# Kernel optimization log

Measured on AMD Instinct MI355X. Metric: run time of the kernel, lower is better.

The kernel has to match this reference:

```python
import jax, jax.numpy as jnp
import numpy as np
from math import sqrt

N, D = 8192, 64

def setup_inputs() -> dict:
    key = jax.random.key(0)
    kq, kk, kv = jax.random.split(key, 3)
    q = jax.random.normal(kq, (N, D), dtype=jnp.float32)
    k = jax.random.normal(kk, (N, D), dtype=jnp.float32)
    v = jax.random.normal(kv, (N, D), dtype=jnp.float32)
    return {"q": q, "k": k, "v": v}

def reference(q, k, v):
    # Mathematically identical to the block-wise online-softmax loop:
    # after processing all KV blocks, m_blk == rowmax(S), l_blk == rowsum(exp(S - m)),
    # O = (exp(S - m) @ V) / l.
    scale = 1.0 / sqrt(q.shape[-1])
    S = (q @ k.T) * scale            # [N, N] attention scores
    m = jnp.max(S, axis=1, keepdims=True)   # running max -> global row max
    P = jnp.exp(S - m)                      # unnormalized probs
    L = jnp.sum(P, axis=1, keepdims=True)   # softmax denominator, [N, 1]
    O = (P @ v) / L                          # [N, D]
    return (O, L)
```

## Files before the change

kernel.cpp:

```cpp
#include <hip/hip_runtime.h>
#include <hip/hip_bf16.h>
#include <math.h>

#define N 8192
#define D 64
#define QSCALE 0.18033688011112042f

typedef __attribute__((ext_vector_type(8))) short short8;
typedef __attribute__((ext_vector_type(16))) float f32x16;

__device__ inline short f32_to_bf16_bits(float x) {
    union { float f; unsigned u; } c; c.f = x;
    unsigned u = c.u;
    u += 0x7FFFu + ((u >> 16) & 1u);
    return (short)(u >> 16);
}
__device__ inline float bfbits_to_f32(unsigned short u) {
    union { unsigned u; float f; } c; c.u = ((unsigned)u) << 16;
    return c.f;
}
__device__ inline unsigned cvt_pk_bf16(float a, float b) {
    __hip_bfloat162 h = __float22bfloat162_rn(make_float2(a, b));
    union { __hip_bfloat162 h; unsigned u; } c; c.h = h;
    return c.u;
}

__global__ __launch_bounds__(256) void fa_conv(const float* __restrict__ q,
                                               const float* __restrict__ k,
                                               const float* __restrict__ v,
                                               short* __restrict__ Qb,
                                               short* __restrict__ Kp,
                                               short* __restrict__ Vp) {
    int bid = blockIdx.x, tid = threadIdx.x;
    if (bid < 512) {
        int i = (bid * 256 + tid) * 4;
        float4 a = *(const float4*)(q + i);
        unsigned lo = cvt_pk_bf16(a.x * QSCALE, a.y * QSCALE);
        unsigned hi = cvt_pk_bf16(a.z * QSCALE, a.w * QSCALE);
        unsigned long long u = (unsigned long long)lo | ((unsigned long long)hi << 32);
        *(unsigned long long*)(Qb + i) = u;
    } else if (bid < 768) {
        int t = bid - 512;
        int c = tid >> 6, l = tid & 63, ql = l & 31, hi = l >> 5;
        const float* src = k + (size_t)(t * 32 + ql) * D + c * 16 + hi * 8;
        float4 a = *(const float4*)(src);
        float4 b = *(const float4*)(src + 4);
        uint4 u = { cvt_pk_bf16(a.x, a.y), cvt_pk_bf16(a.z, a.w),
                    cvt_pk_bf16(b.x, b.y), cvt_pk_bf16(b.z, b.w) };
        *(uint4*)(Kp + (size_t)t * 2048 + c * 512 + ql * 16 + hi * 8) = u;
    } else {
        int t = bid - 768;
        int dt = tid >> 7, h = (tid >> 6) & 1, ql = (tid >> 1) & 31, hi = tid & 1;
        int col = dt * 32 + ql;
        const float* src = v + (size_t)(t * 32 + h * 16 + hi * 8) * D + col;
        float f[8];
#pragma unroll
        for (int j = 0; j < 8; ++j) f[j] = src[(size_t)j * D];
        uint4 u = { cvt_pk_bf16(f[0], f[1]), cvt_pk_bf16(f[2], f[3]),
                    cvt_pk_bf16(f[4], f[5]), cvt_pk_bf16(f[6], f[7]) };
        *(uint4*)(Vp + (size_t)t * 2048 + dt * 1024 + h * 512 + ql * 16 + hi * 8) = u;
    }
}

__global__ __launch_bounds__(256) void fa_part_kernel(const short* __restrict__ Qb,
                                                      const short* __restrict__ Kp,
                                                      const short* __restrict__ Vp,
                                                      short* __restrict__ OTb,
                                                      float* __restrict__ Ml,
                                                      int KN) {
    const int qt = blockIdx.x & 63;
    const int s  = blockIdx.x >> 6;
    const int w = threadIdx.x >> 6, lane = threadIdx.x & 63;
    const int ql = lane & 31, hi = lane >> 5;
    const int qrow = qt * 128 + w * 32 + ql;

    const short* qp = Qb + (size_t)qrow * D + hi * 8;
    short8 qf0 = *(const short8*)(qp);
    short8 qf1 = *(const short8*)(qp + 16);
    short8 qf2 = *(const short8*)(qp + 32);
    short8 qf3 = *(const short8*)(qp + 48);

    f32x16 acc0 = {}, acc1 = {};
    float mex = -INFINITY, lsum = 0.f;

    const int t0 = (s * KN) >> 5, nt = KN >> 5;
    const short* kb = Kp + (size_t)t0 * 2048 + ql * 16 + hi * 8;
    const short* vb = Vp + (size_t)t0 * 2048 + ql * 16 + hi * 8;

#pragma unroll 1
    for (int t = 0; t < nt; ++t) {
        const short* kp = kb + (size_t)t * 2048;
        const short* vp = vb + (size_t)t * 2048;
        short8 kf0  = *(const short8*)(kp);
        short8 kf1  = *(const short8*)(kp + 512);
        short8 kf2  = *(const short8*)(kp + 1024);
        short8 kf3  = *(const short8*)(kp + 1536);
        short8 vf00 = *(const short8*)(vp);
        short8 vf01 = *(const short8*)(vp + 512);
        short8 vf10 = *(const short8*)(vp + 1024);
        short8 vf11 = *(const short8*)(vp + 1536);

        __builtin_amdgcn_s_setprio(1);
        f32x16 st = {};
        st = __builtin_amdgcn_mfma_f32_32x32x16_bf16(kf0, qf0, st, 0, 0, 0);
        st = __builtin_amdgcn_mfma_f32_32x32x16_bf16(kf1, qf1, st, 0, 0, 0);
        st = __builtin_amdgcn_mfma_f32_32x32x16_bf16(kf2, qf2, st, 0, 0, 0);
        st = __builtin_amdgcn_mfma_f32_32x32x16_bf16(kf3, qf3, st, 0, 0, 0);
        __builtin_amdgcn_s_setprio(0);

        float g0 = fmaxf(fmaxf(st[0], st[1]), st[2]);
        float g1 = fmaxf(fmaxf(st[3], st[4]), st[5]);
        float g2 = fmaxf(fmaxf(st[6], st[7]), st[8]);
        float g3 = fmaxf(fmaxf(st[9], st[10]), st[11]);
        float g4 = fmaxf(fmaxf(st[12], st[13]), st[14]);
        float t5 = fmaxf(fmaxf(g0, g1), g2);
        float t6 = fmaxf(fmaxf(g3, g4), st[15]);
        mex = fmaxf(mex, fmaxf(t5, t6));

        unsigned pk0, pk1, pk2, pk3, pk4, pk5, pk6, pk7;
        float rs;
        {
            float a, b;
            a = __builtin_amdgcn_exp2f(st[0]);  b = __builtin_amdgcn_exp2f(st[1]);
            rs = a + b;            pk0 = cvt_pk_bf16(a, b);
            a = __builtin_amdgcn_exp2f(st[2]);  b = __builtin_amdgcn_exp2f(st[3]);
            rs += a + b;           pk1 = cvt_pk_bf16(a, b);
            a = __builtin_amdgcn_exp2f(st[4]);  b = __builtin_amdgcn_exp2f(st[5]);
            rs += a + b;           pk2 = cvt_pk_bf16(a, b);
            a = __builtin_amdgcn_exp2f(st[6]);  b = __builtin_amdgcn_exp2f(st[7]);
            rs += a + b;           pk3 = cvt_pk_bf16(a, b);
            a = __builtin_amdgcn_exp2f(st[8]);  b = __builtin_amdgcn_exp2f(st[9]);
            rs += a + b;           pk4 = cvt_pk_bf16(a, b);
            a = __builtin_amdgcn_exp2f(st[10]); b = __builtin_amdgcn_exp2f(st[11]);
            rs += a + b;           pk5 = cvt_pk_bf16(a, b);
            a = __builtin_amdgcn_exp2f(st[12]); b = __builtin_amdgcn_exp2f(st[13]);
            rs += a + b;           pk6 = cvt_pk_bf16(a, b);
            a = __builtin_amdgcn_exp2f(st[14]); b = __builtin_amdgcn_exp2f(st[15]);
            rs += a + b;           pk7 = cvt_pk_bf16(a, b);
        }
        lsum += rs;

        auto r0 = __builtin_amdgcn_permlane32_swap((int)pk0, (int)pk2, false, false);
        auto r1 = __builtin_amdgcn_permlane32_swap((int)pk1, (int)pk3, false, false);
        auto r2 = __builtin_amdgcn_permlane32_swap((int)pk4, (int)pk6, false, false);
        auto r3 = __builtin_amdgcn_permlane32_swap((int)pk5, (int)pk7, false, false);
        union { int i[4]; short8 s8; } pb0, pb1;
        pb0.i[0] = r0[0]; pb0.i[1] = r1[0]; pb0.i[2] = r0[1]; pb0.i[3] = r1[1];
        pb1.i[0] = r2[0]; pb1.i[1] = r3[0]; pb1.i[2] = r2[1]; pb1.i[3] = r3[1];

        __builtin_amdgcn_s_setprio(1);
        acc0 = __builtin_amdgcn_mfma_f32_32x32x16_bf16(vf00, pb0.s8, acc0, 0, 0, 0);
        acc0 = __builtin_amdgcn_mfma_f32_32x32x16_bf16(vf01, pb1.s8, acc0, 0, 0, 0);
        acc1 = __builtin_amdgcn_mfma_f32_32x32x16_bf16(vf10, pb0.s8, acc1, 0, 0, 0);
        acc1 = __builtin_amdgcn_mfma_f32_32x32x16_bf16(vf11, pb1.s8, acc1, 0, 0, 0);
        __builtin_amdgcn_s_setprio(0);
    }

    mex = fmaxf(mex, __shfl_xor(mex, 32));
    lsum += __shfl_xor(lsum, 32);

#pragma unroll
    for (int r = 0; r < 16; ++r) {
        int d0 = (r & 3) + 8 * (r >> 2) + 4 * hi;
        OTb[(size_t)(s * 64 + d0) * N + qrow]      = f32_to_bf16_bits(acc0[r]);
        OTb[(size_t)(s * 64 + 32 + d0) * N + qrow] = f32_to_bf16_bits(acc1[r]);
    }
    if (hi == 0) {
        Ml[(size_t)(s * 2 + 0) * N + qrow] = lsum;
        Ml[(size_t)(s * 2 + 1) * N + qrow] = mex;
    }
}

__global__ __launch_bounds__(256) void fa_comb_kernel(const short* __restrict__ OTb,
                                                      const float* __restrict__ Ml,
                                                      float* __restrict__ Out, int S) {
    const int r0 = blockIdx.x * 64;
    const int row = threadIdx.x & 63, db = threadIdx.x >> 6;
    const int grow = r0 + row;

    float v[16];
#pragma unroll
    for (int i = 0; i < 16; ++i) v[i] = 0.f;
    float L = 0.f, mg = -INFINITY;
    for (int s = 0; s < S; ++s) {
#pragma unroll
        for (int i = 0; i < 16; ++i)
            v[i] += bfbits_to_f32((unsigned short)OTb[(size_t)(s * 64 + db * 16 + i) * N + grow]);
        L  += Ml[(size_t)(s * 2 + 0) * N + grow];
        mg = fmaxf(mg, Ml[(size_t)(s * 2 + 1) * N + grow]);
    }
    float inv = 1.0f / L;
    float4* outv = (float4*)(Out + (size_t)grow * D + db * 16);
#pragma unroll
    for (int i4 = 0; i4 < 4; ++i4) {
        float4 o = { v[i4 * 4 + 0] * inv, v[i4 * 4 + 1] * inv,
                     v[i4 * 4 + 2] * inv, v[i4 * 4 + 3] * inv };
        outv[i4] = o;
    }
    if (db == 0) Out[(size_t)N * D + grow] = exp2f(-mg) * L;
}

extern "C" void kernel_launch(void* const* d_in, const int* in_sizes, int n_in,
                              void* d_out, int out_size, void* d_ws, size_t ws_size,
                              hipStream_t stream) {
    const float* q = (const float*)d_in[0];
    const float* k = (const float*)d_in[1];
    const float* v = (const float*)d_in[2];
    float* out = (float*)d_out;

    short* Qb = (short*)d_ws;
    short* Kp = Qb + (size_t)N * D;
    short* Vp = Kp + (size_t)N * D;
    short* OTb = (short*)((char*)d_ws + 3 * 1048576);

    int S = 16;
    while (S > 1 &&
           3ull * 1048576 + (size_t)S * (64ull * N * 2) + (size_t)S * (2ull * N * 4) > ws_size)
        S >>= 1;
    float* Ml = (float*)(OTb + (size_t)S * 64 * N);
    int KN = N / S;

    fa_conv<<<1024, 256, 0, stream>>>(q, k, v, Qb, Kp, Vp);
    fa_part_kernel<<<64 * S, 256, 0, stream>>>(Qb, Kp, Vp, OTb, Ml, KN);
    fa_comb_kernel<<<N / 64, 256, 0, stream>>>(OTb, Ml, out, S);
}
```

Baseline: 50.12 us.

## Stage K/V tiles through double-buffered LDS with global_load_lds prefetch

Instead of each wave loading K and V fragments straight from global memory, the block cooperatively copies 64-key K/V tiles into a double-buffered LDS array with global_load_lds, prefetching the next tile while computing on the current one. The conversion kernel's packed layout is changed to a lane-contiguous order so each lane's 16-byte LDS read and each 16-byte global_load_lds line up. The aim is to stop the four waves from each fetching the same K/V data and to hide global latency. In exchange it adds a block-wide barrier and vmcnt wait per tile, uses 32 KB of LDS, and removes the setprio hints.

```diff
diff --git a/kernel.cpp b/kernel.cpp
--- a/kernel.cpp
+++ b/kernel.cpp
@@ -24,6 +24,11 @@
     union { __hip_bfloat162 h; unsigned u; } c; c.h = h;
     return c.u;
 }
+
+#define GLDS(gp, lp)                                                            \
+    __builtin_amdgcn_global_load_lds(                                           \
+        (const __attribute__((address_space(1))) void*)(gp),                    \
+        (__attribute__((address_space(3))) void*)(lp), 16, 0, 0)
 
 __global__ __launch_bounds__(256) void fa_conv(const float* __restrict__ q,
                                                const float* __restrict__ k,
@@ -47,18 +52,17 @@
         float4 b = *(const float4*)(src + 4);
         uint4 u = { cvt_pk_bf16(a.x, a.y), cvt_pk_bf16(a.z, a.w),
                     cvt_pk_bf16(b.x, b.y), cvt_pk_bf16(b.z, b.w) };
-        *(uint4*)(Kp + (size_t)t * 2048 + c * 512 + ql * 16 + hi * 8) = u;
+        *(uint4*)(Kp + (size_t)t * 2048 + c * 512 + l * 8) = u;
     } else {
         int t = bid - 768;
-        int dt = tid >> 7, h = (tid >> 6) & 1, ql = (tid >> 1) & 31, hi = tid & 1;
-        int col = dt * 32 + ql;
-        const float* src = v + (size_t)(t * 32 + h * 16 + hi * 8) * D + col;
+        int dt = tid >> 7, h = (tid >> 6) & 1, hi = (tid >> 5) & 1, ql = tid & 31;
+        const float* src = v + (size_t)(t * 32 + h * 16 + hi * 8) * D + dt * 32 + ql;
         float f[8];
 #pragma unroll
         for (int j = 0; j < 8; ++j) f[j] = src[(size_t)j * D];
         uint4 u = { cvt_pk_bf16(f[0], f[1]), cvt_pk_bf16(f[2], f[3]),
                     cvt_pk_bf16(f[4], f[5]), cvt_pk_bf16(f[6], f[7]) };
-        *(uint4*)(Vp + (size_t)t * 2048 + dt * 1024 + h * 512 + ql * 16 + hi * 8) = u;
+        *(uint4*)(Vp + (size_t)t * 2048 + dt * 1024 + h * 512 + hi * 256 + ql * 8) = u;
     }
 }
 
@@ -68,6 +72,9 @@
                                                       short* __restrict__ OTb,
                                                       float* __restrict__ Ml,
                                                       int KN) {
+    __shared__ short Klds[2][4096];
+    __shared__ short Vlds[2][4096];
+
     const int qt = blockIdx.x & 63;
     const int s  = blockIdx.x >> 6;
     const int w = threadIdx.x >> 6, lane = threadIdx.x & 63;
@@ -83,78 +90,98 @@
     f32x16 acc0 = {}, acc1 = {};
     float mex = -INFINITY, lsum = 0.f;
 
-    const int t0 = (s * KN) >> 5, nt = KN >> 5;
-    const short* kb = Kp + (size_t)t0 * 2048 + ql * 16 + hi * 8;
-    const short* vb = Vp + (size_t)t0 * 2048 + ql * 16 + hi * 8;
+    const int T0 = (s * KN) >> 6, nt = KN >> 6;
+    const short* kg = Kp + (size_t)T0 * 4096 + w * 512 + lane * 8;
+    const short* vg = Vp + (size_t)T0 * 4096 + w * 512 + lane * 8;
+
+#define STAGE(buf, T)                                                     \
+    do {                                                                  \
+        const short* kq = kg + (size_t)(T) * 4096;                        \
+        const short* vq = vg + (size_t)(T) * 4096;                        \
+        GLDS(kq,        &Klds[buf][w * 512]);                             \
+        GLDS(kq + 2048, &Klds[buf][2048 + w * 512]);                      \
+        GLDS(vq,        &Vlds[buf][w * 512]);                             \
+        GLDS(vq + 2048, &Vlds[buf][2048 + w * 512]);                      \
+    } while (0)
+
+    STAGE(0, 0);
+    asm volatile("s_waitcnt vmcnt(0)" ::: "memory");
+    __syncthreads();
 
 #pragma unroll 1
-    for (int t = 0; t < nt; ++t) {
-        const short* kp = kb + (size_t)t * 2048;
-        const short* vp = vb + (size_t)t * 2048;
-        short8 kf0  = *(const short8*)(kp);
-        short8 kf1  = *(const short8*)(kp + 512);
-        short8 kf2  = *(const short8*)(kp + 1024);
-        short8 kf3  = *(const short8*)(kp + 1536);
-        short8 vf00 = *(const short8*)(vp);
-        short8 vf01 = *(const short8*)(vp + 512);
-        short8 vf10 = *(const short8*)(vp + 1024);
-        short8 vf11 = *(const short8*)(vp + 1536);
-
-        __builtin_amdgcn_s_setprio(1);
-        f32x16 st = {};
-        st = __builtin_amdgcn_mfma_f32_32x32x16_bf16(kf0, qf0, st, 0, 0, 0);
-        st = __builtin_amdgcn_mfma_f32_32x32x16_bf16(kf1, qf1, st, 0, 0, 0);
-        st = __builtin_amdgcn_mfma_f32_32x32x16_bf16(kf2, qf2, st, 0, 0, 0);
-        st = __builtin_amdgcn_mfma_f32_32x32x16_bf16(kf3, qf3, st, 0, 0, 0);
-        __builtin_amdgcn_s_setprio(0);
-
-        float g0 = fmaxf(fmaxf(st[0], st[1]), st[2]);
-        float g1 = fmaxf(fmaxf(st[3], st[4]), st[5]);
-        float g2 = fmaxf(fmaxf(st[6], st[7]), st[8]);
-        float g3 = fmaxf(fmaxf(st[9], st[10]), st[11]);
-        float g4 = fmaxf(fmaxf(st[12], st[13]), st[14]);
-        float t5 = fmaxf(fmaxf(g0, g1), g2);
-        float t6 = fmaxf(fmaxf(g3, g4), st[15]);
-        mex = fmaxf(mex, fmaxf(t5, t6));
-
-        unsigned pk0, pk1, pk2, pk3, pk4, pk5, pk6, pk7;
-        float rs;
-        {
-            float a, b;
-            a = __builtin_amdgcn_exp2f(st[0]);  b = __builtin_amdgcn_exp2f(st[1]);
-            rs = a + b;            pk0 = cvt_pk_bf16(a, b);
-            a = __builtin_amdgcn_exp2f(st[2]);  b = __builtin_amdgcn_exp2f(st[3]);
-            rs += a + b;           pk1 = cvt_pk_bf16(a, b);
-            a = __builtin_amdgcn_exp2f(st[4]);  b = __builtin_amdgcn_exp2f(st[5]);
-            rs += a + b;           pk2 = cvt_pk_bf16(a, b);
-            a = __builtin_amdgcn_exp2f(st[6]);  b = __builtin_amdgcn_exp2f(st[7]);
-            rs += a + b;           pk3 = cvt_pk_bf16(a, b);
-            a = __builtin_amdgcn_exp2f(st[8]);  b = __builtin_amdgcn_exp2f(st[9]);
-            rs += a + b;           pk4 = cvt_pk_bf16(a, b);
-            a = __builtin_amdgcn_exp2f(st[10]); b = __builtin_amdgcn_exp2f(st[11]);
-            rs += a + b;           pk5 = cvt_pk_bf16(a, b);
-            a = __builtin_amdgcn_exp2f(st[12]); b = __builtin_amdgcn_exp2f(st[13]);
-            rs += a + b;           pk6 = cvt_pk_bf16(a, b);
-            a = __builtin_amdgcn_exp2f(st[14]); b = __builtin_amdgcn_exp2f(st[15]);
-            rs += a + b;           pk7 = cvt_pk_bf16(a, b);
+    for (int T = 0; T < nt; ++T) {
+        const int cur = T & 1;
+        if (T + 1 < nt) STAGE(cur ^ 1, T + 1);
+
+#pragma unroll
+        for (int u = 0; u < 2; ++u) {
+            const short* kt = &Klds[cur][u * 2048];
+            const short* vt = &Vlds[cur][u * 2048];
+            short8 kf0  = *(const short8*)(kt + lane * 8);
+            short8 kf1  = *(const short8*)(kt + 512 + lane * 8);
+            short8 kf2  = *(const short8*)(kt + 1024 + lane * 8);
+            short8 kf3  = *(const short8*)(kt + 1536 + lane * 8);
+            short8 vf00 = *(const short8*)(vt + lane * 8);
+            short8 vf01 = *(const short8*)(vt + 512 + lane * 8);
+            short8 vf10 = *(const short8*)(vt + 1024 + lane * 8);
+            short8 vf11 = *(const short8*)(vt + 1536 + lane * 8);
+
+            f32x16 st = {};
+            st = __builtin_amdgcn_mfma_f32_32x32x16_bf16(kf0, qf0, st, 0, 0, 0);
+            st = __builtin_amdgcn_mfma_f32_32x32x16_bf16(kf1, qf1, st, 0, 0, 0);
+            st = __builtin_amdgcn_mfma_f32_32x32x16_bf16(kf2, qf2, st, 0, 0, 0);
+            st = __builtin_amdgcn_mfma_f32_32x32x16_bf16(kf3, qf3, st, 0, 0, 0);
+
+            float g0 = fmaxf(fmaxf(st[0], st[1]), st[2]);
+            float g1 = fmaxf(fmaxf(st[3], st[4]), st[5]);
+            float g2 = fmaxf(fmaxf(st[6], st[7]), st[8]);
+            float g3 = fmaxf(fmaxf(st[9], st[10]), st[11]);
+            float g4 = fmaxf(fmaxf(st[12], st[13]), st[14]);
+            float t5 = fmaxf(fmaxf(g0, g1), g2);
+            float t6 = fmaxf(fmaxf(g3, g4), st[15]);
+            mex = fmaxf(mex, fmaxf(t5, t6));
+
+            unsigned pk0, pk1, pk2, pk3, pk4, pk5, pk6, pk7;
+            float rs;
+            {
+                float a, b;
+                a = __builtin_amdgcn_exp2f(st[0]);  b = __builtin_amdgcn_exp2f(st[1]);
+                rs = a + b;            pk0 = cvt_pk_bf16(a, b);
+                a = __builtin_amdgcn_exp2f(st[2]);  b = __builtin_amdgcn_exp2f(st[3]);
+                rs += a + b;           pk1 = cvt_pk_bf16(a, b);
+                a = __builtin_amdgcn_exp2f(st[4]);  b = __builtin_amdgcn_exp2f(st[5]);
+                rs += a + b;           pk2 = cvt_pk_bf16(a, b);
+                a = __builtin_amdgcn_exp2f(st[6]);  b = __builtin_amdgcn_exp2f(st[7]);
+                rs += a + b;           pk3 = cvt_pk_bf16(a, b);
+                a = __builtin_amdgcn_exp2f(st[8]);  b = __builtin_amdgcn_exp2f(st[9]);
+                rs += a + b;           pk4 = cvt_pk_bf16(a, b);
+                a = __builtin_amdgcn_exp2f(st[10]); b = __builtin_amdgcn_exp2f(st[11]);
+                rs += a + b;           pk5 = cvt_pk_bf16(a, b);
+                a = __builtin_amdgcn_exp2f(st[12]); b = __builtin_amdgcn_exp2f(st[13]);
+                rs += a + b;           pk6 = cvt_pk_bf16(a, b);
+                a = __builtin_amdgcn_exp2f(st[14]); b = __builtin_amdgcn_exp2f(st[15]);
+                rs += a + b;           pk7 = cvt_pk_bf16(a, b);
+            }
+            lsum += rs;
+
+            auto r0 = __builtin_amdgcn_permlane32_swap((int)pk0, (int)pk2, false, false);
+            auto r1 = __builtin_amdgcn_permlane32_swap((int)pk1, (int)pk3, false, false);
+            auto r2 = __builtin_amdgcn_permlane32_swap((int)pk4, (int)pk6, false, false);
+            auto r3 = __builtin_amdgcn_permlane32_swap((int)pk5, (int)pk7, false, false);
+            union { int i[4]; short8 s8; } pb0, pb1;
+            pb0.i[0] = r0[0]; pb0.i[1] = r1[0]; pb0.i[2] = r0[1]; pb0.i[3] = r1[1];
+            pb1.i[0] = r2[0]; pb1.i[1] = r3[0]; pb1.i[2] = r2[1]; pb1.i[3] = r3[1];
+
+            acc0 = __builtin_amdgcn_mfma_f32_32x32x16_bf16(vf00, pb0.s8, acc0, 0, 0, 0);
+            acc0 = __builtin_amdgcn_mfma_f32_32x32x16_bf16(vf01, pb1.s8, acc0, 0, 0, 0);
+            acc1 = __builtin_amdgcn_mfma_f32_32x32x16_bf16(vf10, pb0.s8, acc1, 0, 0, 0);
+            acc1 = __builtin_amdgcn_mfma_f32_32x32x16_bf16(vf11, pb1.s8, acc1, 0, 0, 0);
         }
-        lsum += rs;
-
-        auto r0 = __builtin_amdgcn_permlane32_swap((int)pk0, (int)pk2, false, false);
-        auto r1 = __builtin_amdgcn_permlane32_swap((int)pk1, (int)pk3, false, false);
-        auto r2 = __builtin_amdgcn_permlane32_swap((int)pk4, (int)pk6, false, false);
-        auto r3 = __builtin_amdgcn_permlane32_swap((int)pk5, (int)pk7, false, false);
-        union { int i[4]; short8 s8; } pb0, pb1;
-        pb0.i[0] = r0[0]; pb0.i[1] = r1[0]; pb0.i[2] = r0[1]; pb0.i[3] = r1[1];
-        pb1.i[0] = r2[0]; pb1.i[1] = r3[0]; pb1.i[2] = r2[1]; pb1.i[3] = r3[1];
-
-        __builtin_amdgcn_s_setprio(1);
-        acc0 = __builtin_amdgcn_mfma_f32_32x32x16_bf16(vf00, pb0.s8, acc0, 0, 0, 0);
-        acc0 = __builtin_amdgcn_mfma_f32_32x32x16_bf16(vf01, pb1.s8, acc0, 0, 0, 0);
-        acc1 = __builtin_amdgcn_mfma_f32_32x32x16_bf16(vf10, pb0.s8, acc1, 0, 0, 0);
-        acc1 = __builtin_amdgcn_mfma_f32_32x32x16_bf16(vf11, pb1.s8, acc1, 0, 0, 0);
-        __builtin_amdgcn_s_setprio(0);
-    }
+
+        asm volatile("s_waitcnt vmcnt(0)" ::: "memory");
+        __syncthreads();
+    }
+#undef STAGE
 
     mex = fmaxf(mex, __shfl_xor(mex, 32));
     lsum += __shfl_xor(lsum, 32);
```

New measurement: 49.90 us. Within noise of the previous version (-0.4%).

## Prefetch next K tile with double-buffered registers and coalesce packed K/V layout

Applied to the files above, without the earlier changes.

Unrolls the KV loop by two and keeps two register sets for K fragments, so the next tile's K loads are issued before the current tile's MFMAs and softmax run. This is meant to hide global-load latency. The packed K/V layout is changed so each lane reads a contiguous lane*8 offset, which makes the 16-byte loads fully coalesced. The row max now uses v_max3_f32 through inline asm. The cost is more registers, and the loop assumes nt is even.

```diff
diff --git a/kernel.cpp b/kernel.cpp
--- a/kernel.cpp
+++ b/kernel.cpp
@@ -23,6 +23,11 @@
     __hip_bfloat162 h = __float22bfloat162_rn(make_float2(a, b));
     union { __hip_bfloat162 h; unsigned u; } c; c.h = h;
     return c.u;
+}
+__device__ inline float max3f(float a, float b, float c) {
+    float d;
+    asm("v_max3_f32 %0, %1, %2, %3" : "=v"(d) : "v"(a), "v"(b), "v"(c));
+    return d;
 }
 
 __global__ __launch_bounds__(256) void fa_conv(const float* __restrict__ q,
@@ -47,18 +52,17 @@
         float4 b = *(const float4*)(src + 4);
         uint4 u = { cvt_pk_bf16(a.x, a.y), cvt_pk_bf16(a.z, a.w),
                     cvt_pk_bf16(b.x, b.y), cvt_pk_bf16(b.z, b.w) };
-        *(uint4*)(Kp + (size_t)t * 2048 + c * 512 + ql * 16 + hi * 8) = u;
+        *(uint4*)(Kp + (size_t)t * 2048 + c * 512 + l * 8) = u;
     } else {
         int t = bid - 768;
-        int dt = tid >> 7, h = (tid >> 6) & 1, ql = (tid >> 1) & 31, hi = tid & 1;
-        int col = dt * 32 + ql;
-        const float* src = v + (size_t)(t * 32 + h * 16 + hi * 8) * D + col;
+        int dt = tid >> 7, h = (tid >> 6) & 1, hi = (tid >> 5) & 1, ql = tid & 31;
+        const float* src = v + (size_t)(t * 32 + h * 16 + hi * 8) * D + dt * 32 + ql;
         float f[8];
 #pragma unroll
         for (int j = 0; j < 8; ++j) f[j] = src[(size_t)j * D];
         uint4 u = { cvt_pk_bf16(f[0], f[1]), cvt_pk_bf16(f[2], f[3]),
                     cvt_pk_bf16(f[4], f[5]), cvt_pk_bf16(f[6], f[7]) };
-        *(uint4*)(Vp + (size_t)t * 2048 + dt * 1024 + h * 512 + ql * 16 + hi * 8) = u;
+        *(uint4*)(Vp + (size_t)t * 2048 + dt * 1024 + h * 512 + hi * 256 + ql * 8) = u;
     }
 }
 
@@ -84,77 +88,91 @@
     float mex = -INFINITY, lsum = 0.f;
 
     const int t0 = (s * KN) >> 5, nt = KN >> 5;
-    const short* kb = Kp + (size_t)t0 * 2048 + ql * 16 + hi * 8;
-    const short* vb = Vp + (size_t)t0 * 2048 + ql * 16 + hi * 8;
-
+    const short* kbp = Kp + (size_t)t0 * 2048 + lane * 8;
+    const short* vbp = Vp + (size_t)t0 * 2048 + lane * 8;
+
+    short8 kA0, kA1, kA2, kA3, kB0, kB1, kB2, kB3;
+    short8 vf0, vf1, vf2, vf3;
+
+#define LOADK(d0, d1, d2, d3, tt) do {                                     \
+        const short* p_ = kbp + (size_t)(tt) * 2048;                       \
+        d0 = *(const short8*)(p_);                                         \
+        d1 = *(const short8*)(p_ + 512);                                   \
+        d2 = *(const short8*)(p_ + 1024);                                  \
+        d3 = *(const short8*)(p_ + 1536);                                  \
+    } while (0)
+#define LOADV(tt) do {                                                     \
+        const short* p_ = vbp + (size_t)(tt) * 2048;                       \
+        vf0 = *(const short8*)(p_);                                        \
+        vf1 = *(const short8*)(p_ + 512);                                  \
+        vf2 = *(const short8*)(p_ + 1024);                                 \
+        vf3 = *(const short8*)(p_ + 1536);                                 \
+    } while (0)
+
+#define TILE(K0, K1, K2, K3) do {                                           \
+        __builtin_amdgcn_s_setprio(1);                                      \
+        f32x16 st = {};                                                     \
+        st = __builtin_amdgcn_mfma_f32_32x32x16_bf16(K0, qf0, st, 0, 0, 0); \
+        st = __builtin_amdgcn_mfma_f32_32x32x16_bf16(K1, qf1, st, 0, 0, 0); \
+        st = __builtin_amdgcn_mfma_f32_32x32x16_bf16(K2, qf2, st, 0, 0, 0); \
+        st = __builtin_amdgcn_mfma_f32_32x32x16_bf16(K3, qf3, st, 0, 0, 0); \
+        __builtin_amdgcn_s_setprio(0);                                      \
+        float m0_ = max3f(st[0], st[1], st[2]);                             \
+        float m1_ = max3f(st[3], st[4], st[5]);                             \
+        float m2_ = max3f(st[6], st[7], st[8]);                             \
+        float m3_ = max3f(st[9], st[10], st[11]);                           \
+        float m4_ = max3f(st[12], st[13], st[14]);                          \
+        mex = max3f(mex, max3f(m0_, m1_, m2_), max3f(m3_, m4_, st[15]));    \
+        unsigned pk0, pk1, pk2, pk3, pk4, pk5, pk6, pk7;                    \
+        float rs_;                                                          \
+        {                                                                   \
+            float a_, b_;                                                   \
+            a_ = __builtin_amdgcn_exp2f(st[0]);  b_ = __builtin_amdgcn_exp2f(st[1]);  \
+            rs_ = a_ + b_;         pk0 = cvt_pk_bf16(a_, b_);               \
+            a_ = __builtin_amdgcn_exp2f(st[2]);  b_ = __builtin_amdgcn_exp2f(st[3]);  \
+            rs_ += a_ + b_;        pk1 = cvt_pk_bf16(a_, b_);               \
+            a_ = __builtin_amdgcn_exp2f(st[4]);  b_ = __builtin_amdgcn_exp2f(st[5]);  \
+            rs_ += a_ + b_;        pk2 = cvt_pk_bf16(a_, b_);               \
+            a_ = __builtin_amdgcn_exp2f(st[6]);  b_ = __builtin_amdgcn_exp2f(st[7]);  \
+            rs_ += a_ + b_;        pk3 = cvt_pk_bf16(a_, b_);               \
+            a_ = __builtin_amdgcn_exp2f(st[8]);  b_ = __builtin_amdgcn_exp2f(st[9]);  \
+            rs_ += a_ + b_;        pk4 = cvt_pk_bf16(a_, b_);               \
+            a_ = __builtin_amdgcn_exp2f(st[10]); b_ = __builtin_amdgcn_exp2f(st[11]); \
+            rs_ += a_ + b_;        pk5 = cvt_pk_bf16(a_, b_);               \
+            a_ = __builtin_amdgcn_exp2f(st[12]); b_ = __builtin_amdgcn_exp2f(st[13]); \
+            rs_ += a_ + b_;        pk6 = cvt_pk_bf16(a_, b_);               \
+            a_ = __builtin_amdgcn_exp2f(st[14]); b_ = __builtin_amdgcn_exp2f(st[15]); \
+            rs_ += a_ + b_;        pk7 = cvt_pk_bf16(a_, b_);               \
+        }                                                                   \
+        lsum += rs_;                                                        \
+        auto r0_ = __builtin_amdgcn_permlane32_swap((int)pk0, (int)pk2, false, false); \
+        auto r1_ = __builtin_amdgcn_permlane32_swap((int)pk1, (int)pk3, false, false); \
+        auto r2_ = __builtin_amdgcn_permlane32_swap((int)pk4, (int)pk6, false, false); \
+        auto r3_ = __builtin_amdgcn_permlane32_swap((int)pk5, (int)pk7, false, false); \
+        union { int i[4]; short8 s8; } pb0, pb1;                            \
+        pb0.i[0] = r0_[0]; pb0.i[1] = r1_[0]; pb0.i[2] = r0_[1]; pb0.i[3] = r1_[1]; \
+        pb1.i[0] = r2_[0]; pb1.i[1] = r3_[0]; pb1.i[2] = r2_[1]; pb1.i[3] = r3_[1]; \
+        __builtin_amdgcn_s_setprio(1);                                      \
+        acc0 = __builtin_amdgcn_mfma_f32_32x32x16_bf16(vf0, pb0.s8, acc0, 0, 0, 0); \
+        acc0 = __builtin_amdgcn_mfma_f32_32x32x16_bf16(vf1, pb1.s8, acc0, 0, 0, 0); \
+        acc1 = __builtin_amdgcn_mfma_f32_32x32x16_bf16(vf2, pb0.s8, acc1, 0, 0, 0); \
+        acc1 = __builtin_amdgcn_mfma_f32_32x32x16_bf16(vf3, pb1.s8, acc1, 0, 0, 0); \
+        __builtin_amdgcn_s_setprio(0);                                      \
+    } while (0)
+
+    LOADK(kA0, kA1, kA2, kA3, 0);
 #pragma unroll 1
-    for (int t = 0; t < nt; ++t) {
-        const short* kp = kb + (size_t)t * 2048;
-        const short* vp = vb + (size_t)t * 2048;
-        short8 kf0  = *(const short8*)(kp);
-        short8 kf1  = *(const short8*)(kp + 512);
-        short8 kf2  = *(const short8*)(kp + 1024);
-        short8 kf3  = *(const short8*)(kp + 1536);
-        short8 vf00 = *(const short8*)(vp);
-        short8 vf01 = *(const short8*)(vp + 512);
-        short8 vf10 = *(const short8*)(vp + 1024);
-        short8 vf11 = *(const short8*)(vp + 1536);
-
-        __builtin_amdgcn_s_setprio(1);
-        f32x16 st = {};
-        st = __builtin_amdgcn_mfma_f32_32x32x16_bf16(kf0, qf0, st, 0, 0, 0);
-        st = __builtin_amdgcn_mfma_f32_32x32x16_bf16(kf1, qf1, st, 0, 0, 0);
-        st = __builtin_amdgcn_mfma_f32_32x32x16_bf16(kf2, qf2, st, 0, 0, 0);
-        st = __builtin_amdgcn_mfma_f32_32x32x16_bf16(kf3, qf3, st, 0, 0, 0);
-        __builtin_amdgcn_s_setprio(0);
-
-        float g0 = fmaxf(fmaxf(st[0], st[1]), st[2]);
-        float g1 = fmaxf(fmaxf(st[3], st[4]), st[5]);
-        float g2 = fmaxf(fmaxf(st[6], st[7]), st[8]);
-        float g3 = fmaxf(fmaxf(st[9], st[10]), st[11]);
-        float g4 = fmaxf(fmaxf(st[12], st[13]), st[14]);
-        float t5 = fmaxf(fmaxf(g0, g1), g2);
-        float t6 = fmaxf(fmaxf(g3, g4), st[15]);
-        mex = fmaxf(mex, fmaxf(t5, t6));
-
-        unsigned pk0, pk1, pk2, pk3, pk4, pk5, pk6, pk7;
-        float rs;
-        {
-            float a, b;
-            a = __builtin_amdgcn_exp2f(st[0]);  b = __builtin_amdgcn_exp2f(st[1]);
-            rs = a + b;            pk0 = cvt_pk_bf16(a, b);
-            a = __builtin_amdgcn_exp2f(st[2]);  b = __builtin_amdgcn_exp2f(st[3]);
-            rs += a + b;           pk1 = cvt_pk_bf16(a, b);
-            a = __builtin_amdgcn_exp2f(st[4]);  b = __builtin_amdgcn_exp2f(st[5]);
-            rs += a + b;           pk2 = cvt_pk_bf16(a, b);
-            a = __builtin_amdgcn_exp2f(st[6]);  b = __builtin_amdgcn_exp2f(st[7]);
-            rs += a + b;           pk3 = cvt_pk_bf16(a, b);
-            a = __builtin_amdgcn_exp2f(st[8]);  b = __builtin_amdgcn_exp2f(st[9]);
-            rs += a + b;           pk4 = cvt_pk_bf16(a, b);
-            a = __builtin_amdgcn_exp2f(st[10]); b = __builtin_amdgcn_exp2f(st[11]);
-            rs += a + b;           pk5 = cvt_pk_bf16(a, b);
-            a = __builtin_amdgcn_exp2f(st[12]); b = __builtin_amdgcn_exp2f(st[13]);
-            rs += a + b;           pk6 = cvt_pk_bf16(a, b);
-            a = __builtin_amdgcn_exp2f(st[14]); b = __builtin_amdgcn_exp2f(st[15]);
-            rs += a + b;           pk7 = cvt_pk_bf16(a, b);
-        }
-        lsum += rs;
-
-        auto r0 = __builtin_amdgcn_permlane32_swap((int)pk0, (int)pk2, false, false);
-        auto r1 = __builtin_amdgcn_permlane32_swap((int)pk1, (int)pk3, false, false);
-        auto r2 = __builtin_amdgcn_permlane32_swap((int)pk4, (int)pk6, false, false);
-        auto r3 = __builtin_amdgcn_permlane32_swap((int)pk5, (int)pk7, false, false);
-        union { int i[4]; short8 s8; } pb0, pb1;
-        pb0.i[0] = r0[0]; pb0.i[1] = r1[0]; pb0.i[2] = r0[1]; pb0.i[3] = r1[1];
-        pb1.i[0] = r2[0]; pb1.i[1] = r3[0]; pb1.i[2] = r2[1]; pb1.i[3] = r3[1];
-
-        __builtin_amdgcn_s_setprio(1);
-        acc0 = __builtin_amdgcn_mfma_f32_32x32x16_bf16(vf00, pb0.s8, acc0, 0, 0, 0);
-        acc0 = __builtin_amdgcn_mfma_f32_32x32x16_bf16(vf01, pb1.s8, acc0, 0, 0, 0);
-        acc1 = __builtin_amdgcn_mfma_f32_32x32x16_bf16(vf10, pb0.s8, acc1, 0, 0, 0);
-        acc1 = __builtin_amdgcn_mfma_f32_32x32x16_bf16(vf11, pb1.s8, acc1, 0, 0, 0);
-        __builtin_amdgcn_s_setprio(0);
-    }
+    for (int T = 0; T < nt; T += 2) {
+        LOADV(T);
+        LOADK(kB0, kB1, kB2, kB3, T + 1);
+        TILE(kA0, kA1, kA2, kA3);
+        LOADV(T + 1);
+        if (T + 2 < nt) LOADK(kA0, kA1, kA2, kA3, T + 2);
+        TILE(kB0, kB1, kB2, kB3);
+    }
+#undef LOADK
+#undef LOADV
+#undef TILE
 
     mex = fmaxf(mex, __shfl_xor(mex, 32));
     lsum += __shfl_xor(lsum, 32);
```

Result: faster. 48.61 us (-3.0%).
